# Kernel tuning notes

Hardware: AMD Instinct MI355X
Metric: run time of the kernel (lower is better)

The kernel has to match this reference:

```python
import jax, jax.numpy as jnp
import numpy as np

N, C, O, R, T, V = 128, 64, 64, 8, 128, 25  # batch, in_ch, out_ch, rel_ch, frames, joints
EPS = 1e-5


def _c1(x, w, b):
    # 1x1 conv2d over channel dim: x [n,i,t,v], w [o,i], b [o]
    return jnp.einsum('oi,nitv->notv', w, x) + b[None, :, None, None]


def _tconv(x, w):
    # temporal conv, kernel [3,1], pad [1,0]: x [n,c,t,1], w [o,i,3,1]
    return jax.lax.conv_general_dilated(
        x, w, window_strides=(1, 1), padding=((1, 1), (0, 0)),
        dimension_numbers=('NCHW', 'OIHW', 'NCHW'))


def setup_inputs() -> dict:
    key = jax.random.key(0)
    ks = jax.random.split(key, 16)
    d = {}
    d['x'] = jax.random.normal(ks[0], (N, C, T, V), jnp.float32)
    d['A'] = jax.random.normal(ks[1], (V, V), jnp.float32) * 0.1
    d['alpha'] = jnp.ones((1,), jnp.float32)
    s_c = 1.0 / np.sqrt(C)
    s_r = 1.0 / np.sqrt(R)
    d['w1'] = jax.random.normal(ks[2], (R, C), jnp.float32) * s_c
    d['b1'] = jnp.zeros((R,), jnp.float32)
    d['w2'] = jax.random.normal(ks[3], (R, C), jnp.float32) * s_c
    d['b2'] = jnp.zeros((R,), jnp.float32)
    d['w5'] = jax.random.normal(ks[4], (R, C), jnp.float32) * s_c
    d['b5'] = jnp.zeros((R,), jnp.float32)
    d['w3'] = jax.random.normal(ks[5], (O, R), jnp.float32) * s_r
    d['b3'] = jnp.zeros((O,), jnp.float32)
    d['w4'] = jax.random.normal(ks[6], (O, R), jnp.float32) * s_r
    d['b4'] = jnp.zeros((O,), jnp.float32)
    # RouteFuncMLP params (ratio=1, kernels=[3,3])
    d['g_w'] = jax.random.normal(ks[7], (R, R), jnp.float32) * s_r
    d['g_b'] = jnp.zeros((R,), jnp.float32)
    d['a_w'] = jax.random.normal(ks[8], (R, R, 3, 1), jnp.float32) * s_r
    d['a_b'] = jnp.zeros((R,), jnp.float32)
    d['bn_g'] = jnp.ones((R,), jnp.float32)
    d['bn_b'] = jnp.zeros((R,), jnp.float32)
    d['bn_rm'] = jnp.zeros((R,), jnp.float32)
    d['bn_rv'] = jnp.ones((R,), jnp.float32)
    # conv_rf.b is zero-init in torch (trivial gate); randomize small for a meaningful test
    d['rf_bw'] = jax.random.normal(ks[9], (R, R, 3, 1), jnp.float32) * 0.05
    return d


def reference(x, A, alpha, w1, b1, w2, b2, w5, b5, w3, b3, w4, b4,
              g_w, g_b, a_w, a_b, bn_g, bn_b, bn_rm, bn_rv, rf_bw):
    # x1, x2: 1x1 conv then mean over T  -> [N,R,V]
    x1 = _c1(x, w1, b1).mean(axis=2)
    x2 = _c1(x, w2, b2).mean(axis=2)
    x3 = _c1(x, w5, b5)  # [N,R,T,V]

    # RouteFuncMLP gating on x3
    g = x3.mean(axis=(2, 3), keepdims=True)          # global pool [N,R,1,1]
    p = x3.mean(axis=3, keepdims=True)               # pool over V [N,R,T,1]
    gg = _c1(g, g_w, g_b)                            # 1x1 conv on global pool
    h = _tconv(p + gg, a_w) + a_b[None, :, None, None]
    h = (h - bn_rm[None, :, None, None]) * (bn_g / jnp.sqrt(bn_rv + EPS))[None, :, None, None] + bn_b[None, :, None, None]
    h = jax.nn.relu(h)
    rf = _tconv(h, rf_bw) + 1.0                      # [N,R,T,1]

    x3 = _c1(x3 * rf, w3, b3)                        # [N,O,T,V]

    # relation tensor: broadcast diff + tanh -> [N,R,V,V]
    rel = jnp.tanh(x1[:, :, :, None] - x2[:, :, None, :])
    rel = _c1(rel, w4, b4) * alpha[0] + A[None, None]  # [N,O,V,V]

    # aggregation: out[n,c,t,u] = sum_v rel[n,c,u,v] * x3[n,c,t,v]
    out = jnp.einsum('ncuv,nctv->nctu', rel, x3)
    return out
```

## Files before the change

kernel.cpp:

```cpp
#include <hip/hip_runtime.h>

#define N_ 128
#define C_ 64
#define O_ 64
#define R_ 8
#define T_ 128
#define V_ 25
#define TV_ 3200
#define EPS_ 1e-5f
#define G_ 8

__global__ __launch_bounds__(256) void k1_colsum(const float* __restrict__ x,
                                                 float* __restrict__ S) {
    int ni = blockIdx.x;
    const float* xp = x + (size_t)ni * TV_;
    int tid = threadIdx.x;
    __shared__ float part[200];
    if (tid < 200) {
        float s = 0.f;
        #pragma unroll
        for (int k = 0; k < 16; ++k) s += xp[tid + 200 * k];
        part[tid] = s;
    }
    __syncthreads();
    if (tid < V_) {
        float t = 0.f;
        #pragma unroll
        for (int g = 0; g < 8; ++g) t += part[g * 25 + tid];
        S[ni * V_ + tid] = t;
    }
}

__global__ __launch_bounds__(256) void k3_x3(const float* __restrict__ x,
        const float* __restrict__ w5, const float* __restrict__ b5,
        float* __restrict__ x3) {
    int gid = blockIdx.x * 256 + threadIdx.x;
    int n = gid / TV_, p = gid % TV_;
    float acc[R_];
    #pragma unroll
    for (int r = 0; r < R_; ++r) acc[r] = b5[r];
    const float* xp = x + (size_t)n * C_ * TV_ + p;
    #pragma unroll
    for (int i = 0; i < C_; ++i) {
        float xv = xp[(size_t)i * TV_];
        #pragma unroll
        for (int r = 0; r < R_; ++r) acc[r] += w5[r * C_ + i] * xv;
    }
    float* x3p = x3 + (size_t)n * R_ * TV_ + p;
    #pragma unroll
    for (int r = 0; r < R_; ++r) x3p[(size_t)r * TV_] = acc[r];
}

__global__ __launch_bounds__(256) void k2_rel(const float* __restrict__ S,
        const float* __restrict__ w1, const float* __restrict__ b1,
        const float* __restrict__ w2, const float* __restrict__ b2,
        const float* __restrict__ w4, const float* __restrict__ b4,
        const float* __restrict__ A, const float* __restrict__ alpha,
        float* __restrict__ rel2) {
    int n = blockIdx.x, og = blockIdx.y;
    int c0 = og * 16;
    int tid = threadIdx.x;
    __shared__ float x1s[R_ * V_];
    __shared__ float x2s[R_ * V_];
    __shared__ float rels[R_ * 625];
    const float invT = 1.0f / (float)T_;
    for (int idx = tid; idx < 2 * R_ * V_; idx += 256) {
        int s = idx / (R_ * V_), rv = idx % (R_ * V_);
        int r = rv / V_, v = rv % V_;
        const float* w = s ? w2 : w1;
        float a = 0.f;
        for (int i = 0; i < C_; ++i) a += w[r * C_ + i] * S[(n * C_ + i) * V_ + v];
        a = a * invT + (s ? b2[r] : b1[r]);
        (s ? x2s : x1s)[rv] = a;
    }
    __syncthreads();
    for (int idx = tid; idx < R_ * 625; idx += 256) {
        int r = idx / 625, uv = idx % 625;
        rels[idx] = tanhf(x1s[r * V_ + uv / V_] - x2s[r * V_ + uv % V_]);
    }
    __syncthreads();
    float al = alpha[0];
    for (int idx = tid; idx < 16 * 625; idx += 256) {
        int o = c0 + idx / 625, uv = idx % 625;
        float acc = b4[o];
        #pragma unroll
        for (int r = 0; r < R_; ++r) acc += w4[o * R_ + r] * rels[r * 625 + uv];
        rel2[((size_t)n * O_ + o) * 625 + uv] = acc * al + A[uv];
    }
}

__global__ __launch_bounds__(256) void kP_pool(const float* __restrict__ x3,
                                               float* __restrict__ ppool) {
    int nr = blockIdx.x;
    int tid = threadIdx.x;
    __shared__ float buf[TV_];
    const float* xp = x3 + (size_t)nr * TV_;
    for (int idx = tid; idx < TV_; idx += 256) buf[idx] = xp[idx];
    __syncthreads();
    if (tid < T_) {
        float s = 0.f;
        #pragma unroll
        for (int v = 0; v < V_; ++v) s += buf[tid * V_ + v];
        ppool[(size_t)nr * T_ + tid] = s;
    }
}

__global__ __launch_bounds__(256) void k4b_route(const float* __restrict__ ppool,
        const float* __restrict__ g_w, const float* __restrict__ g_b,
        const float* __restrict__ a_w, const float* __restrict__ a_b,
        const float* __restrict__ bn_g, const float* __restrict__ bn_b,
        const float* __restrict__ bn_rm, const float* __restrict__ bn_rv,
        const float* __restrict__ rf_bw, float* __restrict__ rf) {
    int n = blockIdx.x, th = blockIdx.y;
    int t0 = th * 64;
    int tid = threadIdx.x;
    __shared__ float ps[R_][T_];
    __shared__ float hs[R_][68];
    __shared__ float ggs[R_];
    for (int idx = tid; idx < R_ * T_; idx += 256)
        ps[idx / T_][idx % T_] = ppool[(size_t)n * R_ * T_ + idx] * (1.0f / V_);
    __syncthreads();
    if (tid < R_) {
        float s = 0.f;
        for (int t = 0; t < T_; ++t) s += ps[tid][t];
        hs[tid][0] = s * (1.0f / T_);
    }
    __syncthreads();
    if (tid < R_) {
        float a = g_b[tid];
        #pragma unroll
        for (int i = 0; i < R_; ++i) a += g_w[tid * R_ + i] * hs[i][0];
        ggs[tid] = a;
    }
    __syncthreads();
    for (int idx = tid; idx < R_ * 66; idx += 256) {
        int r = idx / 66, j = idx % 66;
        int t = t0 + j - 1;
        float h = 0.f;
        if (t >= 0 && t < T_) {
            float acc = a_b[r];
            #pragma unroll
            for (int i = 0; i < R_; ++i) {
                #pragma unroll
                for (int k = 0; k < 3; ++k) {
                    int tt = t + k - 1;
                    if (tt >= 0 && tt < T_)
                        acc += a_w[(r * R_ + i) * 3 + k] * (ps[i][tt] + ggs[i]);
                }
            }
            float sc = bn_g[r] * rsqrtf(bn_rv[r] + EPS_);
            h = fmaxf((acc - bn_rm[r]) * sc + bn_b[r], 0.f);
        }
        hs[r][j + 1] = h;
    }
    __syncthreads();
    for (int idx = tid; idx < R_ * 64; idx += 256) {
        int r = idx / 64, j = idx % 64;
        int t = t0 + j;
        float acc = 1.0f;
        #pragma unroll
        for (int i = 0; i < R_; ++i) {
            #pragma unroll
            for (int k = 0; k < 3; ++k) {
                int tt = t + k - 1;
                if (tt >= 0 && tt < T_)
                    acc += rf_bw[(r * R_ + i) * 3 + k] * hs[i][j + k + 1];
            }
        }
        rf[((size_t)n * R_ + r) * T_ + t] = acc;
    }
}

__global__ __launch_bounds__(512) void k5_out(const float* __restrict__ x3,
        const float* __restrict__ rf, const float* __restrict__ rel2,
        const float* __restrict__ w3, const float* __restrict__ b3,
        float* __restrict__ out) {
    int b = blockIdx.x;
    int n = b / 16;
    int rem = b % 16;
    int cg = rem / 2, th = rem % 2;
    int c0 = cg * G_;
    int tid = threadIdx.x;
    __shared__ float rfs[R_][64];
    __shared__ __align__(16) float zs[G_][1600];
    {
        int r = tid / 64, tl = tid % 64;
        rfs[r][tl] = rf[((size_t)n * R_ + r) * T_ + th * 64 + tl];
    }
    __syncthreads();
    const float* x3p = x3 + (size_t)n * R_ * TV_ + th * 1600;
    for (int p = tid; p < 1600; p += 512) {
        int t = p / V_;
        float y[R_];
        #pragma unroll
        for (int r = 0; r < R_; ++r) y[r] = x3p[(size_t)r * TV_ + p] * rfs[r][t];
        #pragma unroll
        for (int cl = 0; cl < G_; ++cl) {
            float a = b3[c0 + cl];
            #pragma unroll
            for (int r = 0; r < R_; ++r) a += w3[(c0 + cl) * R_ + r] * y[r];
            zs[cl][p] = a;
        }
    }
    __syncthreads();
    {
        int cl = __builtin_amdgcn_readfirstlane(tid >> 6);
        int tl = tid & 63;
        const float* relp = rel2 + ((size_t)n * O_ + c0 + cl) * 625;
        float zreg[V_];
        #pragma unroll
        for (int v = 0; v < V_; ++v) zreg[v] = zs[cl][tl * V_ + v];
        float accu[V_];
        #pragma unroll
        for (int u = 0; u < V_; ++u) {
            float acc = 0.f;
            #pragma unroll
            for (int j = 0; j < V_; ++j) acc += relp[u * V_ + j] * zreg[j];
            accu[u] = acc;
        }
        #pragma unroll
        for (int u = 0; u < V_; ++u) zs[cl][tl * V_ + u] = accu[u];
    }
    __syncthreads();
    size_t ob = (((size_t)n * O_ + c0) * T_ + th * 64) * V_;
    float4* out4 = (float4*)(out + ob);
    const float4* zf4 = (const float4*)&zs[0][0];
    for (int j = tid; j < 3200; j += 512) {
        int cl = j / 400, r4 = j % 400;
        out4[(size_t)cl * 800 + r4] = zf4[j];
    }
}

extern "C" void kernel_launch(void* const* d_in, const int* in_sizes, int n_in,
                              void* d_out, int out_size, void* d_ws, size_t ws_size,
                              hipStream_t stream) {
    const float* x     = (const float*)d_in[0];
    const float* A     = (const float*)d_in[1];
    const float* alpha = (const float*)d_in[2];
    const float* w1    = (const float*)d_in[3];
    const float* b1    = (const float*)d_in[4];
    const float* w2    = (const float*)d_in[5];
    const float* b2    = (const float*)d_in[6];
    const float* w5    = (const float*)d_in[7];
    const float* b5    = (const float*)d_in[8];
    const float* w3    = (const float*)d_in[9];
    const float* b3    = (const float*)d_in[10];
    const float* w4    = (const float*)d_in[11];
    const float* b4    = (const float*)d_in[12];
    const float* g_w   = (const float*)d_in[13];
    const float* g_b   = (const float*)d_in[14];
    const float* a_w   = (const float*)d_in[15];
    const float* a_b   = (const float*)d_in[16];
    const float* bn_g  = (const float*)d_in[17];
    const float* bn_b  = (const float*)d_in[18];
    const float* bn_rm = (const float*)d_in[19];
    const float* bn_rv = (const float*)d_in[20];
    const float* rf_bw = (const float*)d_in[21];
    float* out = (float*)d_out;
    float* ws  = (float*)d_ws;

    float* S     = ws;
    float* x3    = S + 204800;
    float* ppool = x3 + 3276800;
    float* rf    = ppool + 131072;
    float* rel2  = rf + 131072;

    hipLaunchKernelGGL(k1_colsum, dim3(N_ * C_), dim3(256), 0, stream, x, S);
    hipLaunchKernelGGL(k3_x3, dim3(1600), dim3(256), 0, stream, x, w5, b5, x3);
    hipLaunchKernelGGL(k2_rel, dim3(N_, 4), dim3(256), 0, stream,
                       S, w1, b1, w2, b2, w4, b4, A, alpha, rel2);
    hipLaunchKernelGGL(kP_pool, dim3(N_ * R_), dim3(256), 0, stream, x3, ppool);
    hipLaunchKernelGGL(k4b_route, dim3(N_, 2), dim3(256), 0, stream,
                       ppool, g_w, g_b, a_w, a_b, bn_g, bn_b, bn_rm, bn_rv, rf_bw, rf);
    hipLaunchKernelGGL(k5_out, dim3(N_ * 16), dim3(512), 0, stream,
                       x3, rf, rel2, w3, b3, out);
}
```

Measured before the change: 318.0 us.

## Fuse front-end kernels into one x-pass and merge rel/route kernels

Replaces the separate column-sum, x3 projection, and pooling kernels with a single kernel that reads x once. It computes x3 and accumulates the V-pooled sums and the w1/w2-projected T-sums through shared-memory atomics. The relation and route-gating kernels are merged into one launch, with the route work placed in an extra blockIdx.y slice. The output kernel remaps block indices so each XCD handles distinct batches. This removes a second full read of x, a reread of x3 for pooling, and two launches, at the cost of shared atomics and low occupancy in the fused kernel.

```diff
diff --git a/kernel.cpp b/kernel.cpp
--- a/kernel.cpp
+++ b/kernel.cpp
@@ -10,134 +10,114 @@
 #define EPS_ 1e-5f
 #define G_ 8
 
-__global__ __launch_bounds__(256) void k1_colsum(const float* __restrict__ x,
-                                                 float* __restrict__ S) {
-    int ni = blockIdx.x;
-    const float* xp = x + (size_t)ni * TV_;
+__global__ __launch_bounds__(256) void kA(const float* __restrict__ x,
+        const float* __restrict__ w5, const float* __restrict__ b5,
+        const float* __restrict__ w1, const float* __restrict__ w2,
+        float* __restrict__ x3, float* __restrict__ x12p, float* __restrict__ ppool) {
+    int n = blockIdx.x, y = blockIdx.y;
     int tid = threadIdx.x;
-    __shared__ float part[200];
-    if (tid < 200) {
-        float s = 0.f;
-        #pragma unroll
-        for (int k = 0; k < 16; ++k) s += xp[tid + 200 * k];
-        part[tid] = s;
-    }
-    __syncthreads();
-    if (tid < V_) {
-        float t = 0.f;
-        #pragma unroll
-        for (int g = 0; g < 8; ++g) t += part[g * 25 + tid];
-        S[ni * V_ + tid] = t;
-    }
-}
-
-__global__ __launch_bounds__(256) void k3_x3(const float* __restrict__ x,
-        const float* __restrict__ w5, const float* __restrict__ b5,
-        float* __restrict__ x3) {
-    int gid = blockIdx.x * 256 + threadIdx.x;
-    int n = gid / TV_, p = gid % TV_;
-    float acc[R_];
+    bool act = tid < 200;
+    int g = tid / 25, v = tid % 25;
+    __shared__ __align__(16) float wls[C_][24];
+    __shared__ float ppart[R_][16];
+    __shared__ float s12part[16][25];
+    for (int idx = tid; idx < C_ * 24; idx += 256) {
+        int i = idx / 24, r = idx % 24;
+        wls[i][r] = (r < 8) ? w5[r * C_ + i]
+                  : (r < 16) ? w1[(r - 8) * C_ + i]
+                             : w2[(r - 16) * C_ + i];
+    }
+    for (int idx = tid; idx < R_ * 16; idx += 256) (&ppart[0][0])[idx] = 0.f;
+    for (int idx = tid; idx < 16 * 25; idx += 256) (&s12part[0][0])[idx] = 0.f;
+    __syncthreads();
+
+    float acc0[R_], acc1[R_], s12[16];
     #pragma unroll
-    for (int r = 0; r < R_; ++r) acc[r] = b5[r];
-    const float* xp = x + (size_t)n * C_ * TV_ + p;
+    for (int r = 0; r < R_; ++r) { acc0[r] = 0.f; acc1[r] = 0.f; }
     #pragma unroll
-    for (int i = 0; i < C_; ++i) {
-        float xv = xp[(size_t)i * TV_];
-        #pragma unroll
-        for (int r = 0; r < R_; ++r) acc[r] += w5[r * C_ + i] * xv;
-    }
-    float* x3p = x3 + (size_t)n * R_ * TV_ + p;
-    #pragma unroll
-    for (int r = 0; r < R_; ++r) x3p[(size_t)r * TV_] = acc[r];
-}
-
-__global__ __launch_bounds__(256) void k2_rel(const float* __restrict__ S,
-        const float* __restrict__ w1, const float* __restrict__ b1,
-        const float* __restrict__ w2, const float* __restrict__ b2,
+    for (int rr = 0; rr < 16; ++rr) s12[rr] = 0.f;
+
+    if (act) {
+        int off0 = (g + 16 * y) * 25 + v;
+        const float* xp = x + (size_t)n * C_ * TV_;
+        #pragma unroll 2
+        for (int i = 0; i < C_; ++i) {
+            float xv0 = xp[(size_t)i * TV_ + off0];
+            float xv1 = xp[(size_t)i * TV_ + off0 + 200];
+            const float4* wp = (const float4*)&wls[i][0];
+            float4 q0 = wp[0], q1 = wp[1];
+            float4 q2 = wp[2], q3 = wp[3];
+            float4 q4 = wp[4], q5 = wp[5];
+            acc0[0] += q0.x * xv0; acc0[1] += q0.y * xv0; acc0[2] += q0.z * xv0; acc0[3] += q0.w * xv0;
+            acc0[4] += q1.x * xv0; acc0[5] += q1.y * xv0; acc0[6] += q1.z * xv0; acc0[7] += q1.w * xv0;
+            acc1[0] += q0.x * xv1; acc1[1] += q0.y * xv1; acc1[2] += q0.z * xv1; acc1[3] += q0.w * xv1;
+            acc1[4] += q1.x * xv1; acc1[5] += q1.y * xv1; acc1[6] += q1.z * xv1; acc1[7] += q1.w * xv1;
+            float xs = xv0 + xv1;
+            s12[0]  += q2.x * xs; s12[1]  += q2.y * xs; s12[2]  += q2.z * xs; s12[3]  += q2.w * xs;
+            s12[4]  += q3.x * xs; s12[5]  += q3.y * xs; s12[6]  += q3.z * xs; s12[7]  += q3.w * xs;
+            s12[8]  += q4.x * xs; s12[9]  += q4.y * xs; s12[10] += q4.z * xs; s12[11] += q4.w * xs;
+            s12[12] += q5.x * xs; s12[13] += q5.y * xs; s12[14] += q5.z * xs; s12[15] += q5.w * xs;
+        }
+        float* x3p = x3 + (size_t)n * R_ * TV_;
+        #pragma unroll
+        for (int r = 0; r < R_; ++r) {
+            float v0 = acc0[r] + b5[r];
+            float v1 = acc1[r] + b5[r];
+            x3p[(size_t)r * TV_ + off0]       = v0;
+            x3p[(size_t)r * TV_ + off0 + 200] = v1;
+            atomicAdd(&ppart[r][g], v0);
+            atomicAdd(&ppart[r][g + 8], v1);
+        }
+        #pragma unroll
+        for (int rr = 0; rr < 16; ++rr) atomicAdd(&s12part[rr][v], s12[rr]);
+    }
+    __syncthreads();
+    if (tid < 128) {
+        int r = tid / 16, tl = tid % 16;
+        ppool[((size_t)n * R_ + r) * T_ + 16 * y + tl] = ppart[r][tl];
+    }
+    for (int idx = tid; idx < 400; idx += 256)
+        x12p[((size_t)n * 8 + y) * 400 + idx] = (&s12part[0][0])[idx];
+}
+
+__global__ __launch_bounds__(256) void kB(const float* __restrict__ x12p,
+        const float* __restrict__ b1, const float* __restrict__ b2,
         const float* __restrict__ w4, const float* __restrict__ b4,
         const float* __restrict__ A, const float* __restrict__ alpha,
-        float* __restrict__ rel2) {
-    int n = blockIdx.x, og = blockIdx.y;
-    int c0 = og * 16;
-    int tid = threadIdx.x;
-    __shared__ float x1s[R_ * V_];
-    __shared__ float x2s[R_ * V_];
-    __shared__ float rels[R_ * 625];
-    const float invT = 1.0f / (float)T_;
-    for (int idx = tid; idx < 2 * R_ * V_; idx += 256) {
-        int s = idx / (R_ * V_), rv = idx % (R_ * V_);
-        int r = rv / V_, v = rv % V_;
-        const float* w = s ? w2 : w1;
-        float a = 0.f;
-        for (int i = 0; i < C_; ++i) a += w[r * C_ + i] * S[(n * C_ + i) * V_ + v];
-        a = a * invT + (s ? b2[r] : b1[r]);
-        (s ? x2s : x1s)[rv] = a;
-    }
-    __syncthreads();
-    for (int idx = tid; idx < R_ * 625; idx += 256) {
-        int r = idx / 625, uv = idx % 625;
-        rels[idx] = tanhf(x1s[r * V_ + uv / V_] - x2s[r * V_ + uv % V_]);
-    }
-    __syncthreads();
-    float al = alpha[0];
-    for (int idx = tid; idx < 16 * 625; idx += 256) {
-        int o = c0 + idx / 625, uv = idx % 625;
-        float acc = b4[o];
-        #pragma unroll
-        for (int r = 0; r < R_; ++r) acc += w4[o * R_ + r] * rels[r * 625 + uv];
-        rel2[((size_t)n * O_ + o) * 625 + uv] = acc * al + A[uv];
-    }
-}
-
-__global__ __launch_bounds__(256) void kP_pool(const float* __restrict__ x3,
-                                               float* __restrict__ ppool) {
-    int nr = blockIdx.x;
-    int tid = threadIdx.x;
-    __shared__ float buf[TV_];
-    const float* xp = x3 + (size_t)nr * TV_;
-    for (int idx = tid; idx < TV_; idx += 256) buf[idx] = xp[idx];
-    __syncthreads();
-    if (tid < T_) {
-        float s = 0.f;
-        #pragma unroll
-        for (int v = 0; v < V_; ++v) s += buf[tid * V_ + v];
-        ppool[(size_t)nr * T_ + tid] = s;
-    }
-}
-
-__global__ __launch_bounds__(256) void k4b_route(const float* __restrict__ ppool,
+        const float* __restrict__ ppool,
         const float* __restrict__ g_w, const float* __restrict__ g_b,
         const float* __restrict__ a_w, const float* __restrict__ a_b,
         const float* __restrict__ bn_g, const float* __restrict__ bn_b,
         const float* __restrict__ bn_rm, const float* __restrict__ bn_rv,
-        const float* __restrict__ rf_bw, float* __restrict__ rf) {
-    int n = blockIdx.x, th = blockIdx.y;
-    int t0 = th * 64;
-    int tid = threadIdx.x;
-    __shared__ float ps[R_][T_];
-    __shared__ float hs[R_][68];
-    __shared__ float ggs[R_];
-    for (int idx = tid; idx < R_ * T_; idx += 256)
-        ps[idx / T_][idx % T_] = ppool[(size_t)n * R_ * T_ + idx] * (1.0f / V_);
-    __syncthreads();
-    if (tid < R_) {
-        float s = 0.f;
-        for (int t = 0; t < T_; ++t) s += ps[tid][t];
-        hs[tid][0] = s * (1.0f / T_);
-    }
-    __syncthreads();
-    if (tid < R_) {
-        float a = g_b[tid];
-        #pragma unroll
-        for (int i = 0; i < R_; ++i) a += g_w[tid * R_ + i] * hs[i][0];
-        ggs[tid] = a;
-    }
-    __syncthreads();
-    for (int idx = tid; idx < R_ * 66; idx += 256) {
-        int r = idx / 66, j = idx % 66;
-        int t = t0 + j - 1;
-        float h = 0.f;
-        if (t >= 0 && t < T_) {
+        const float* __restrict__ rf_bw,
+        float* __restrict__ rel2, float* __restrict__ rf) {
+    int n = blockIdx.x, tid = threadIdx.x;
+    if (blockIdx.y == 4) {
+        __shared__ float ps[R_][T_];
+        __shared__ float hsx[R_][T_ + 2];
+        __shared__ float gs[R_], ggs[R_];
+        for (int idx = tid; idx < R_ * T_; idx += 256)
+            ps[idx / T_][idx % T_] = ppool[(size_t)n * R_ * T_ + idx] * (1.0f / V_);
+        if (tid < R_ * 2) {
+            int r = tid / 2;
+            hsx[r][(tid % 2) * (T_ + 1)] = 0.f;
+        }
+        __syncthreads();
+        if (tid < R_) {
+            float s = 0.f;
+            for (int t = 0; t < T_; ++t) s += ps[tid][t];
+            gs[tid] = s * (1.0f / T_);
+        }
+        __syncthreads();
+        if (tid < R_) {
+            float a = g_b[tid];
+            #pragma unroll
+            for (int i = 0; i < R_; ++i) a += g_w[tid * R_ + i] * gs[i];
+            ggs[tid] = a;
+        }
+        __syncthreads();
+        for (int idx = tid; idx < R_ * T_; idx += 256) {
+            int r = idx / T_, t = idx % T_;
             float acc = a_b[r];
             #pragma unroll
             for (int i = 0; i < R_; ++i) {
@@ -149,25 +129,48 @@
                 }
             }
             float sc = bn_g[r] * rsqrtf(bn_rv[r] + EPS_);
-            h = fmaxf((acc - bn_rm[r]) * sc + bn_b[r], 0.f);
-        }
-        hs[r][j + 1] = h;
-    }
-    __syncthreads();
-    for (int idx = tid; idx < R_ * 64; idx += 256) {
-        int r = idx / 64, j = idx % 64;
-        int t = t0 + j;
-        float acc = 1.0f;
-        #pragma unroll
-        for (int i = 0; i < R_; ++i) {
-            #pragma unroll
-            for (int k = 0; k < 3; ++k) {
-                int tt = t + k - 1;
-                if (tt >= 0 && tt < T_)
-                    acc += rf_bw[(r * R_ + i) * 3 + k] * hs[i][j + k + 1];
+            hsx[r][t + 1] = fmaxf((acc - bn_rm[r]) * sc + bn_b[r], 0.f);
+        }
+        __syncthreads();
+        for (int idx = tid; idx < R_ * T_; idx += 256) {
+            int r = idx / T_, t = idx % T_;
+            float acc = 1.0f;
+            #pragma unroll
+            for (int i = 0; i < R_; ++i) {
+                #pragma unroll
+                for (int k = 0; k < 3; ++k)
+                    acc += rf_bw[(r * R_ + i) * 3 + k] * hsx[i][t + k];
             }
-        }
-        rf[((size_t)n * R_ + r) * T_ + t] = acc;
+            rf[((size_t)n * R_ + r) * T_ + t] = acc;
+        }
+        return;
+    }
+    int c0 = blockIdx.y * 16;
+    __shared__ float x1s[R_ * V_];
+    __shared__ float x2s[R_ * V_];
+    __shared__ float rels[R_ * 625];
+    const float invT = 1.0f / (float)T_;
+    for (int idx = tid; idx < 400; idx += 256) {
+        int rr = idx / 25;
+        float a = 0.f;
+        #pragma unroll
+        for (int b = 0; b < 8; ++b) a += x12p[((size_t)n * 8 + b) * 400 + idx];
+        a = a * invT + ((rr < 8) ? b1[rr] : b2[rr - 8]);
+        if (rr < 8) x1s[idx] = a; else x2s[idx - 200] = a;
+    }
+    __syncthreads();
+    for (int idx = tid; idx < R_ * 625; idx += 256) {
+        int r = idx / 625, uv = idx % 625;
+        rels[idx] = tanhf(x1s[r * V_ + uv / V_] - x2s[r * V_ + uv % V_]);
+    }
+    __syncthreads();
+    float al = alpha[0];
+    for (int idx = tid; idx < 16 * 625; idx += 256) {
+        int o = c0 + idx / 625, uv = idx % 625;
+        float acc = b4[o];
+        #pragma unroll
+        for (int r = 0; r < R_; ++r) acc += w4[o * R_ + r] * rels[r * 625 + uv];
+        rel2[((size_t)n * O_ + o) * 625 + uv] = acc * al + A[uv];
     }
 }
 
@@ -176,9 +179,10 @@
         const float* __restrict__ w3, const float* __restrict__ b3,
         float* __restrict__ out) {
     int b = blockIdx.x;
-    int n = b / 16;
-    int rem = b % 16;
-    int cg = rem / 2, th = rem % 2;
+    int xcd = b & 7, slot = b >> 3;
+    int n = (slot >> 4) * 8 + xcd;
+    int rem = slot & 15;
+    int cg = rem >> 1, th = rem & 1;
     int c0 = cg * G_;
     int tid = threadIdx.x;
     __shared__ float rfs[R_][64];
@@ -259,19 +263,18 @@
     float* out = (float*)d_out;
     float* ws  = (float*)d_ws;
 
-    float* S     = ws;
-    float* x3    = S + 204800;
-    float* ppool = x3 + 3276800;
+    float* x3    = ws;
+    float* x12p  = x3 + 3276800;
+    float* ppool = x12p + 409600;
     float* rf    = ppool + 131072;
     float* rel2  = rf + 131072;
 
-    hipLaunchKernelGGL(k1_colsum, dim3(N_ * C_), dim3(256), 0, stream, x, S);
-    hipLaunchKernelGGL(k3_x3, dim3(1600), dim3(256), 0, stream, x, w5, b5, x3);
-    hipLaunchKernelGGL(k2_rel, dim3(N_, 4), dim3(256), 0, stream,
-                       S, w1, b1, w2, b2, w4, b4, A, alpha, rel2);
-    hipLaunchKernelGGL(kP_pool, dim3(N_ * R_), dim3(256), 0, stream, x3, ppool);
-    hipLaunchKernelGGL(k4b_route, dim3(N_, 2), dim3(256), 0, stream,
-                       ppool, g_w, g_b, a_w, a_b, bn_g, bn_b, bn_rm, bn_rv, rf_bw, rf);
+    hipLaunchKernelGGL(kA, dim3(N_, 8), dim3(256), 0, stream,
+                       x, w5, b5, w1, w2, x3, x12p, ppool);
+    hipLaunchKernelGGL(kB, dim3(N_, 5), dim3(256), 0, stream,
+                       x12p, b1, b2, w4, b4, A, alpha,
+                       ppool, g_w, g_b, a_w, a_b, bn_g, bn_b, bn_rm, bn_rv, rf_bw,
+                       rel2, rf);
     hipLaunchKernelGGL(k5_out, dim3(N_ * 16), dim3(512), 0, stream,
                        x3, rf, rel2, w3, b3, out);
 }
```

Result: no change. 318.2 us (+0.1%).
